# Kernel tuning notes

Hardware: AMD Instinct MI355X
Metric: run time of the kernel (lower is better)

Reference implementation:

```python
import jax, jax.numpy as jnp
import numpy as np
from jax import lax

N, E, F, H, B = 16384, 262144, 32, 128, 16
DI, DS, DC, DTR = 256, 16, 4, 8   # Mamba: d_inner=expand*H, d_state, d_conv, dt_rank=ceil(H/16)
NS, NC = 512, 8                   # num_stations, num line colors
EPS = 1e-5


def _forward(node_features, edge_index, batch, W_in, b_in, W_g1, b_g1, W_g2, b_g2,
             W_inproj, conv_w, conv_b, W_xproj, W_dt, b_dt, A_log, D_p, W_out,
             gamma, beta, Wc, bc, Wh, bh, Wt, bt, Wp1, bp1, Wp2, bp2, Wd, bd, Ws, bs):
    def gcn(x, W, b):
        # GCNConv with self-loops and symmetric normalization
        loops = jnp.arange(N)
        s = jnp.concatenate([edge_index[0], loops])
        d = jnp.concatenate([edge_index[1], loops])
        deg = jax.ops.segment_sum(jnp.ones(s.shape[0], x.dtype), d, num_segments=N)
        dinv = jnp.where(deg > 0, lax.rsqrt(deg), 0.0)
        xw = x @ W
        msg = xw[s] * (dinv[s] * dinv[d])[:, None]
        return jax.ops.segment_sum(msg, d, num_segments=N) + b

    h = jax.nn.relu(node_features @ W_in + b_in)
    h = jax.nn.relu(gcn(h, W_g1, b_g1))
    h_gnn = jax.nn.relu(gcn(h, W_g2, b_g2))

    # --- Mamba block over the node sequence (batch dim of 1, seq_len = N) ---
    xz = h_gnn @ W_inproj                      # (N, 2*DI)
    x, z = xz[:, :DI], xz[:, DI:]
    xp = jnp.pad(x, ((DC - 1, 0), (0, 0)))     # causal depthwise conv1d
    xc = conv_b + sum(xp[k:k + N] * conv_w[:, k] for k in range(DC))
    x = jax.nn.silu(xc)
    dbl = x @ W_xproj                          # (N, DTR + 2*DS)
    dt = jax.nn.softplus(dbl[:, :DTR] @ W_dt + b_dt)   # (N, DI)
    Bm = dbl[:, DTR:DTR + DS]                  # (N, DS)
    Cm = dbl[:, DTR + DS:]                     # (N, DS)
    A = -jnp.exp(A_log)                        # (DI, DS)
    dA = jnp.exp(dt[:, :, None] * A[None])     # (N, DI, DS)
    dBx = dt[:, :, None] * Bm[:, None, :] * x[:, :, None]

    def step(hst, t):
        dA_t, dBx_t, C_t = t
        hst = dA_t * hst + dBx_t               # (DI, DS)
        return hst, hst @ C_t                  # (DI,)

    _, ys = lax.scan(step, jnp.zeros((DI, DS), x.dtype), (dA, dBx, Cm))
    y = (ys + D_p * x) * jax.nn.silu(z)
    h_mamba = y @ W_out                        # (N, H)

    # residual + LayerNorm
    hh = h_gnn + h_mamba
    mu = hh.mean(-1, keepdims=True)
    var = ((hh - mu) ** 2).mean(-1, keepdims=True)
    h_final = (hh - mu) * lax.rsqrt(var + EPS) * gamma + beta

    # global_mean_pool per graph
    counts = jax.ops.segment_sum(jnp.ones(N, h_final.dtype), batch, num_segments=B)
    ge = jax.ops.segment_sum(h_final, batch, num_segments=B) / jnp.maximum(counts, 1.0)[:, None]

    # critic + all policy heads, concatenated: [1,4,3,NS,NS,NS,NC]
    return jnp.concatenate([ge @ Wc + bc, ge @ Wh + bh, ge @ Wt + bt,
                            ge @ Wp1 + bp1, ge @ Wp2 + bp2, ge @ Wd + bd,
                            ge @ Ws + bs], axis=-1)


def setup_inputs() -> dict:
    key = jax.random.key(0)
    ks = list(jax.random.split(key, 20))
    p = lambda i, shape, s=0.02: jax.random.normal(ks[i], shape, jnp.float32) * s
    return dict(
        node_features=jax.random.normal(ks[0], (N, F), jnp.float32),
        edge_index=jax.random.randint(ks[1], (2, E), 0, N),
        batch=jnp.sort(jax.random.randint(ks[2], (N,), 0, B)),
        W_in=p(3, (F, H)), b_in=jnp.zeros((H,), jnp.float32),
        W_g1=p(4, (H, H)), b_g1=jnp.zeros((H,), jnp.float32),
        W_g2=p(5, (H, H)), b_g2=jnp.zeros((H,), jnp.float32),
        W_inproj=p(6, (H, 2 * DI)),
        conv_w=p(7, (DI, DC)), conv_b=jnp.zeros((DI,), jnp.float32),
        W_xproj=p(8, (DI, DTR + 2 * DS)),
        W_dt=p(9, (DTR, DI)), b_dt=jnp.full((DI,), -4.0, jnp.float32),
        A_log=jnp.log(jnp.broadcast_to(jnp.arange(1.0, DS + 1.0, dtype=jnp.float32), (DI, DS))),
        D_p=jnp.ones((DI,), jnp.float32),
        W_out=p(10, (DI, H)),
        gamma=jnp.ones((H,), jnp.float32), beta=jnp.zeros((H,), jnp.float32),
        Wc=p(11, (H, 1)), bc=jnp.zeros((1,), jnp.float32),
        Wh=p(12, (H, 4)), bh=jnp.zeros((4,), jnp.float32),
        Wt=p(13, (H, 3)), bt=jnp.zeros((3,), jnp.float32),
        Wp1=p(14, (H, NS)), bp1=jnp.zeros((NS,), jnp.float32),
        Wp2=p(15, (H, NS)), bp2=jnp.zeros((NS,), jnp.float32),
        Wd=p(16, (H, NS)), bd=jnp.zeros((NS,), jnp.float32),
        Ws=p(17, (H, NC)), bs=jnp.zeros((NC,), jnp.float32),
    )


def reference(node_features, edge_index, batch, W_in, b_in, W_g1, b_g1, W_g2, b_g2,
              W_inproj, conv_w, conv_b, W_xproj, W_dt, b_dt, A_log, D_p, W_out,
              gamma, beta, Wc, bc, Wh, bh, Wt, bt, Wp1, bp1, Wp2, bp2, Wd, bd, Ws, bs):
    return _forward(node_features, edge_index, batch, W_in, b_in, W_g1, b_g1, W_g2, b_g2,
                    W_inproj, conv_w, conv_b, W_xproj, W_dt, b_dt, A_log, D_p, W_out,
                    gamma, beta, Wc, bc, Wh, bh, Wt, bt, Wp1, bp1, Wp2, bp2, Wd, bd, Ws, bs)
```

## Files before the change

### kernel.cpp

```cpp
#include <hip/hip_runtime.h>
#include <math.h>

#define NN 16384
#define EE 262144
#define FF 32
#define HH 128
#define BB 16
#define DI 256
#define DS 16
#define DC 4
#define DTR 8
#define OUTW 1552
#define NCH 256
#define CHLEN 64
#define NG 8
#define GL 32

__device__ __forceinline__ float siluf(float v) { return v / (1.f + __expf(-v)); }
__device__ __forceinline__ float softplusf(float v) {
    return fmaxf(v, 0.f) + __logf(1.f + __expf(-fabsf(v)));
}

__global__ void deg_kernel(const int* __restrict__ dst, int* __restrict__ cnt) {
    int e = blockIdx.x * blockDim.x + threadIdx.x;
    if (e < EE) atomicAdd(&cnt[dst[e]], 1);
}

__global__ __launch_bounds__(1024) void prefix_kernel(const int* __restrict__ cnt,
                                                      int* __restrict__ rowptr,
                                                      int* __restrict__ cursor,
                                                      float* __restrict__ dinv) {
    __shared__ int part[1024];
    int tid = threadIdx.x;
    int4 c4[4];
#pragma unroll
    for (int j = 0; j < 4; j++) c4[j] = ((const int4*)cnt)[tid * 4 + j];
    int v[16] = {c4[0].x, c4[0].y, c4[0].z, c4[0].w, c4[1].x, c4[1].y, c4[1].z, c4[1].w,
                 c4[2].x, c4[2].y, c4[2].z, c4[2].w, c4[3].x, c4[3].y, c4[3].z, c4[3].w};
    int s = 0;
#pragma unroll
    for (int j = 0; j < 16; j++) s += v[j];
    part[tid] = s;
    __syncthreads();
    for (int off = 1; off < 1024; off <<= 1) {
        int t = (tid >= off) ? part[tid - off] : 0;
        __syncthreads();
        part[tid] += t;
        __syncthreads();
    }
    int running = part[tid] - s;
    int rp[16];
    float dv[16];
#pragma unroll
    for (int j = 0; j < 16; j++) {
        rp[j] = running;
        running += v[j];
        dv[j] = rsqrtf((float)(v[j] + 1));
    }
#pragma unroll
    for (int j = 0; j < 4; j++) {
        int4 r4; r4.x = rp[j*4]; r4.y = rp[j*4+1]; r4.z = rp[j*4+2]; r4.w = rp[j*4+3];
        ((int4*)rowptr)[tid * 4 + j] = r4;
        ((int4*)cursor)[tid * 4 + j] = r4;
        float4 d4; d4.x = dv[j*4]; d4.y = dv[j*4+1]; d4.z = dv[j*4+2]; d4.w = dv[j*4+3];
        ((float4*)dinv)[tid * 4 + j] = d4;
    }
    if (tid == 1023) rowptr[NN] = part[1023];
}

__global__ void scatter_kernel(const int* __restrict__ src, const int* __restrict__ dst,
                               int* __restrict__ cursor, int* __restrict__ col) {
    int e = blockIdx.x * blockDim.x + threadIdx.x;
    if (e < EE) {
        int d = dst[e];
        int pos = atomicAdd(&cursor[d], 1);
        col[pos] = src[e];
    }
}

__global__ __launch_bounds__(256) void gemm_k(const float* __restrict__ A,
                                              const float* __restrict__ B,
                                              const float* __restrict__ bias,
                                              float* __restrict__ C,
                                              int M, int Nn, int K, int act) {
    __shared__ float As[16][68];
    __shared__ float Bs[16][68];
    int tid = threadIdx.x;
    int m0 = blockIdx.y * 64;
    int n0 = blockIdx.x * 64;
    int ty = tid >> 4, tx = tid & 15;
    float acc[4][4] = {{0.f}};
    for (int k0 = 0; k0 < K; k0 += 16) {
#pragma unroll
        for (int l = 0; l < 4; l++) {
            int idx = tid + l * 256;
            int i = idx >> 4, j = idx & 15;
            As[j][i] = A[(size_t)(m0 + i) * K + k0 + j];
        }
#pragma unroll
        for (int l = 0; l < 4; l++) {
            int idx = tid + l * 256;
            int i = idx >> 6, j = idx & 63;
            int n = n0 + j;
            Bs[i][j] = (n < Nn) ? B[(size_t)(k0 + i) * Nn + n] : 0.f;
        }
        __syncthreads();
#pragma unroll
        for (int kk = 0; kk < 16; kk++) {
            float4 a4 = *(const float4*)&As[kk][ty * 4];
            float4 b4 = *(const float4*)&Bs[kk][tx * 4];
            float av[4] = {a4.x, a4.y, a4.z, a4.w};
            float bv[4] = {b4.x, b4.y, b4.z, b4.w};
#pragma unroll
            for (int r = 0; r < 4; r++)
#pragma unroll
                for (int c = 0; c < 4; c++) acc[r][c] = fmaf(av[r], bv[c], acc[r][c]);
        }
        __syncthreads();
    }
    int nb = n0 + tx * 4;
    if (nb < Nn) {
        float4 bi4 = {0.f, 0.f, 0.f, 0.f};
        if (bias) bi4 = *(const float4*)&bias[nb];
#pragma unroll
        for (int r = 0; r < 4; r++) {
            int m = m0 + ty * 4 + r;
            float4 v;
            v.x = acc[r][0] + bi4.x; v.y = acc[r][1] + bi4.y;
            v.z = acc[r][2] + bi4.z; v.w = acc[r][3] + bi4.w;
            if (act == 1) {
                v.x = fmaxf(v.x, 0.f); v.y = fmaxf(v.y, 0.f);
                v.z = fmaxf(v.z, 0.f); v.w = fmaxf(v.w, 0.f);
            }
            *(float4*)&C[(size_t)m * Nn + nb] = v;
        }
    }
}

__global__ __launch_bounds__(256, 4) void gemm_big(const float* __restrict__ A,
                                                   const float* __restrict__ B,
                                                   float* __restrict__ C,
                                                   int M, int Nn, int K) {
    __shared__ float As[16][132];
    __shared__ float Bs[16][132];
    int tid = threadIdx.x;
    int m0 = blockIdx.y * 128;
    int n0 = blockIdx.x * 128;
    int ty = tid >> 4, tx = tid & 15;
    float acc[8][8] = {{0.f}};
    for (int k0 = 0; k0 < K; k0 += 16) {
        {
            int m = tid >> 1;
            int kc = (tid & 1) * 8;
            const float* ap = &A[(size_t)(m0 + m) * K + k0 + kc];
            float4 a0 = *(const float4*)ap;
            float4 a1 = *(const float4*)(ap + 4);
            As[kc + 0][m] = a0.x; As[kc + 1][m] = a0.y;
            As[kc + 2][m] = a0.z; As[kc + 3][m] = a0.w;
            As[kc + 4][m] = a1.x; As[kc + 5][m] = a1.y;
            As[kc + 6][m] = a1.z; As[kc + 7][m] = a1.w;
        }
        {
            int krow = tid >> 4;
            int c8 = (tid & 15) * 8;
            const float* bp = &B[(size_t)(k0 + krow) * Nn + n0 + c8];
            *(float4*)&Bs[krow][c8] = *(const float4*)bp;
            *(float4*)&Bs[krow][c8 + 4] = *(const float4*)(bp + 4);
        }
        __syncthreads();
#pragma unroll
        for (int kk = 0; kk < 16; kk++) {
            float4 a0 = *(const float4*)&As[kk][ty * 4];
            float4 a1 = *(const float4*)&As[kk][64 + ty * 4];
            float4 b0 = *(const float4*)&Bs[kk][tx * 4];
            float4 b1 = *(const float4*)&Bs[kk][64 + tx * 4];
            float av[8] = {a0.x, a0.y, a0.z, a0.w, a1.x, a1.y, a1.z, a1.w};
            float bv[8] = {b0.x, b0.y, b0.z, b0.w, b1.x, b1.y, b1.z, b1.w};
#pragma unroll
            for (int r = 0; r < 8; r++)
#pragma unroll
                for (int c = 0; c < 8; c++) acc[r][c] = fmaf(av[r], bv[c], acc[r][c]);
        }
        __syncthreads();
    }
#pragma unroll
    for (int r = 0; r < 8; r++) {
        int m = m0 + ((r < 4) ? (ty * 4 + r) : (64 + ty * 4 + r - 4));
        float4 v0, v1;
        v0.x = acc[r][0]; v0.y = acc[r][1]; v0.z = acc[r][2]; v0.w = acc[r][3];
        v1.x = acc[r][4]; v1.y = acc[r][5]; v1.z = acc[r][6]; v1.w = acc[r][7];
        *(float4*)&C[(size_t)m * Nn + n0 + tx * 4] = v0;
        *(float4*)&C[(size_t)m * Nn + n0 + 64 + tx * 4] = v1;
    }
}

__global__ __launch_bounds__(256) void gemm_at(const float* __restrict__ AT,
                                               const float* __restrict__ B,
                                               float* __restrict__ C,
                                               int M, int Nn, int K) {
    __shared__ float As[16][68];
    __shared__ float Bs[16][68];
    int tid = threadIdx.x;
    int m0 = blockIdx.y * 64;
    int n0 = blockIdx.x * 64;
    int ty = tid >> 4, tx = tid & 15;
    float acc[4][4] = {{0.f}};
    for (int k0 = 0; k0 < K; k0 += 16) {
#pragma unroll
        for (int l = 0; l < 4; l++) {
            int idx = tid + l * 256;
            int kk = idx >> 6, i = idx & 63;
            As[kk][i] = AT[(size_t)(k0 + kk) * M + m0 + i];
        }
#pragma unroll
        for (int l = 0; l < 4; l++) {
            int idx = tid + l * 256;
            int i = idx >> 6, j = idx & 63;
            int n = n0 + j;
            Bs[i][j] = (n < Nn) ? B[(size_t)(k0 + i) * Nn + n] : 0.f;
        }
        __syncthreads();
#pragma unroll
        for (int kk = 0; kk < 16; kk++) {
            float4 a4 = *(const float4*)&As[kk][ty * 4];
            float4 b4 = *(const float4*)&Bs[kk][tx * 4];
            float av[4] = {a4.x, a4.y, a4.z, a4.w};
            float bv[4] = {b4.x, b4.y, b4.z, b4.w};
#pragma unroll
            for (int r = 0; r < 4; r++)
#pragma unroll
                for (int c = 0; c < 4; c++) acc[r][c] = fmaf(av[r], bv[c], acc[r][c]);
        }
        __syncthreads();
    }
    int nb = n0 + tx * 4;
    if (nb < Nn) {
#pragma unroll
        for (int r = 0; r < 4; r++) {
            int m = m0 + ty * 4 + r;
            float4 v;
            v.x = acc[r][0]; v.y = acc[r][1]; v.z = acc[r][2]; v.w = acc[r][3];
            *(float4*)&C[(size_t)m * Nn + nb] = v;
        }
    }
}

__global__ __launch_bounds__(256) void gemm_at_ln(const float* __restrict__ AT,
                                                  const float* __restrict__ B,
                                                  const float* __restrict__ hg,
                                                  const float* __restrict__ gamma,
                                                  const float* __restrict__ beta,
                                                  float* __restrict__ out) {
    __shared__ float As[16][68];
    __shared__ float Bs[16][132];
    int tid = threadIdx.x;
    int m0 = blockIdx.x * 64;
    int ty = tid >> 4, tx = tid & 15;
    float acc[4][8] = {{0.f}};
    for (int k0 = 0; k0 < 256; k0 += 16) {
#pragma unroll
        for (int l = 0; l < 4; l++) {
            int idx = tid + l * 256;
            int kk = idx >> 6, i = idx & 63;
            As[kk][i] = AT[(size_t)(k0 + kk) * NN + m0 + i];
        }
        {
            int krow = tid >> 4;
            int c8 = (tid & 15) * 8;
            const float* bp = &B[(size_t)(k0 + krow) * HH + c8];
            *(float4*)&Bs[krow][c8] = *(const float4*)bp;
            *(float4*)&Bs[krow][c8 + 4] = *(const float4*)(bp + 4);
        }
        __syncthreads();
#pragma unroll
        for (int kk = 0; kk < 16; kk++) {
            float4 a4 = *(const float4*)&As[kk][ty * 4];
            float4 b0 = *(const float4*)&Bs[kk][tx * 4];
            float4 b1 = *(const float4*)&Bs[kk][64 + tx * 4];
            float av[4] = {a4.x, a4.y, a4.z, a4.w};
            float bv[8] = {b0.x, b0.y, b0.z, b0.w, b1.x, b1.y, b1.z, b1.w};
#pragma unroll
            for (int r = 0; r < 4; r++)
#pragma unroll
                for (int c = 0; c < 8; c++) acc[r][c] = fmaf(av[r], bv[c], acc[r][c]);
        }
        __syncthreads();
    }
    float4 g0 = *(const float4*)&gamma[tx * 4];
    float4 g1 = *(const float4*)&gamma[64 + tx * 4];
    float4 be0 = *(const float4*)&beta[tx * 4];
    float4 be1 = *(const float4*)&beta[64 + tx * 4];
    float gv[8] = {g0.x, g0.y, g0.z, g0.w, g1.x, g1.y, g1.z, g1.w};
    float bv[8] = {be0.x, be0.y, be0.z, be0.w, be1.x, be1.y, be1.z, be1.w};
#pragma unroll
    for (int r = 0; r < 4; r++) {
        int m = m0 + ty * 4 + r;
        float4 h0 = *(const float4*)&hg[(size_t)m * HH + tx * 4];
        float4 h1 = *(const float4*)&hg[(size_t)m * HH + 64 + tx * 4];
        float v[8] = {acc[r][0] + h0.x, acc[r][1] + h0.y, acc[r][2] + h0.z, acc[r][3] + h0.w,
                      acc[r][4] + h1.x, acc[r][5] + h1.y, acc[r][6] + h1.z, acc[r][7] + h1.w};
        float sum = 0.f;
#pragma unroll
        for (int c = 0; c < 8; c++) sum += v[c];
        sum += __shfl_xor(sum, 1); sum += __shfl_xor(sum, 2);
        sum += __shfl_xor(sum, 4); sum += __shfl_xor(sum, 8);
        float mu = sum * (1.f / 128.f);
        float vs = 0.f;
#pragma unroll
        for (int c = 0; c < 8; c++) { float dd = v[c] - mu; vs += dd * dd; }
        vs += __shfl_xor(vs, 1); vs += __shfl_xor(vs, 2);
        vs += __shfl_xor(vs, 4); vs += __shfl_xor(vs, 8);
        float inv = rsqrtf(vs * (1.f / 128.f) + 1e-5f);
        float4 o0, o1;
        o0.x = (v[0] - mu) * inv * gv[0] + bv[0];
        o0.y = (v[1] - mu) * inv * gv[1] + bv[1];
        o0.z = (v[2] - mu) * inv * gv[2] + bv[2];
        o0.w = (v[3] - mu) * inv * gv[3] + bv[3];
        o1.x = (v[4] - mu) * inv * gv[4] + bv[4];
        o1.y = (v[5] - mu) * inv * gv[5] + bv[5];
        o1.z = (v[6] - mu) * inv * gv[6] + bv[6];
        o1.w = (v[7] - mu) * inv * gv[7] + bv[7];
        *(float4*)&out[(size_t)m * HH + tx * 4] = o0;
        *(float4*)&out[(size_t)m * HH + 64 + tx * 4] = o1;
    }
}

__global__ __launch_bounds__(256) void gcn_gather4(const float* __restrict__ xw,
                                                   const int* __restrict__ rowptr,
                                                   const int* __restrict__ col,
                                                   const float* __restrict__ dinv,
                                                   const float* __restrict__ b,
                                                   float* __restrict__ out) {
    int tid = threadIdx.x;
    int sub = tid & 31;
    int n = blockIdx.x * 8 + (tid >> 5);
    float dn = dinv[n];
    const float4* xw4 = (const float4*)xw;
    float4 a = xw4[(size_t)n * 32 + sub];
    float ws = dn * dn;
    float4 acc;
    acc.x = a.x * ws; acc.y = a.y * ws; acc.z = a.z * ws; acc.w = a.w * ws;
    int beg = rowptr[n], end = rowptr[n + 1];
    int e = beg;
    for (; e + 2 <= end; e += 2) {
        int s0 = col[e], s1 = col[e + 1];
        float w0 = dinv[s0] * dn, w1 = dinv[s1] * dn;
        float4 v0 = xw4[(size_t)s0 * 32 + sub];
        float4 v1 = xw4[(size_t)s1 * 32 + sub];
        acc.x = fmaf(v0.x, w0, acc.x); acc.y = fmaf(v0.y, w0, acc.y);
        acc.z = fmaf(v0.z, w0, acc.z); acc.w = fmaf(v0.w, w0, acc.w);
        acc.x = fmaf(v1.x, w1, acc.x); acc.y = fmaf(v1.y, w1, acc.y);
        acc.z = fmaf(v1.z, w1, acc.z); acc.w = fmaf(v1.w, w1, acc.w);
    }
    if (e < end) {
        int s0 = col[e];
        float w0 = dinv[s0] * dn;
        float4 v0 = xw4[(size_t)s0 * 32 + sub];
        acc.x = fmaf(v0.x, w0, acc.x); acc.y = fmaf(v0.y, w0, acc.y);
        acc.z = fmaf(v0.z, w0, acc.z); acc.w = fmaf(v0.w, w0, acc.w);
    }
    float4 b4 = ((const float4*)b)[sub];
    acc.x = fmaxf(acc.x + b4.x, 0.f);
    acc.y = fmaxf(acc.y + b4.y, 0.f);
    acc.z = fmaxf(acc.z + b4.z, 0.f);
    acc.w = fmaxf(acc.w + b4.w, 0.f);
    ((float4*)out)[(size_t)n * 32 + sub] = acc;
}

__global__ __launch_bounds__(256) void conv_silu_t(const float* __restrict__ xz,
                                                   const float* __restrict__ cw,
                                                   const float* __restrict__ cb,
                                                   float* __restrict__ xst,
                                                   float* __restrict__ szt) {
    __shared__ float tile[67][65];
    int tid = threadIdx.x;
    int t0 = blockIdx.x * 64;
    int c0 = blockIdx.y * 64;
#pragma unroll
    for (int l = 0; l < 17; l++) {
        int idx = tid + l * 256;
        if (idx < 67 * 64) {
            int r = idx >> 6, c = idx & 63;
            int gt = t0 - 3 + r;
            tile[r][c] = (gt >= 0) ? xz[(size_t)gt * 512 + c0 + c] : 0.f;
        }
    }
    __syncthreads();
    int tl = tid & 63;
    int d0 = tid >> 6;
    if (c0 < 256) {
#pragma unroll
        for (int l = 0; l < 16; l++) {
            int dl = d0 + l * 4;
            int dg = c0 + dl;
            float acc = cb[dg];
#pragma unroll
            for (int k = 0; k < DC; k++)
                acc = fmaf(tile[tl + k][dl], cw[dg * DC + k], acc);
            xst[dg * NN + t0 + tl] = siluf(acc);
        }
    } else {
#pragma unroll
        for (int l = 0; l < 16; l++) {
            int dl = d0 + l * 4;
            int dg = c0 - 256 + dl;
            szt[dg * NN + t0 + tl] = siluf(tile[tl + 3][dl]);
        }
    }
}

__global__ __launch_bounds__(256) void transpose_dbl(const float* __restrict__ dbl,
                                                     float* __restrict__ dblt) {
    __shared__ float tile[64][41];
    int tid = threadIdx.x;
    int t0 = blockIdx.x * 64;
#pragma unroll
    for (int l = 0; l < 10; l++) {
        int idx = tid + l * 256;
        int r = idx / 40, c = idx - r * 40;
        tile[r][c] = dbl[(size_t)(t0 + r) * 40 + c];
    }
    __syncthreads();
#pragma unroll
    for (int l = 0; l < 10; l++) {
        int idx = tid + l * 256;
        int c = idx >> 6, t = idx & 63;
        dblt[c * NN + t0 + t] = tile[t][c];
    }
}

__global__ __launch_bounds__(256, 6) void scan_phase1(const float* __restrict__ xst,
                                                      const float* __restrict__ dblt,
                                                      const float* __restrict__ A_log,
                                                      const float* __restrict__ W_dt,
                                                      const float* __restrict__ b_dt,
                                                      float* __restrict__ chkP,
                                                      float* __restrict__ chkH) {
    __shared__ float Td[32][68];
    __shared__ float Tx[32][68];
    __shared__ float Bs[16][68];
    __shared__ float D8[8][68];
    int tid = threadIdx.x;
    int wave = tid >> 6, lane = tid & 63;
    int sg = lane & 7, dl = lane >> 3;
    int dblk = blockIdx.x, chunk = blockIdx.y;
    int t0 = chunk * CHLEN;
    int dloc = wave * 8 + dl;
    int d = dblk * 32 + dloc;
    int s0 = 2 * sg;
#pragma unroll
    for (int p = 0; p < 2; p++) {
        int linear = tid + p * 256;
        int row = linear >> 4, c4 = (linear & 15) * 4;
        *(float4*)&Tx[row][c4] = *(const float4*)&xst[(size_t)(dblk * 32 + row) * NN + t0 + c4];
    }
    if (tid < 128) {
        int r = tid >> 4, c4 = (tid & 15) * 4;
        *(float4*)&D8[r][c4] = *(const float4*)&dblt[(size_t)r * NN + t0 + c4];
    }
    {
        int s = tid >> 4, c4 = (tid & 15) * 4;
        *(float4*)&Bs[s][c4] = *(const float4*)&dblt[(size_t)(8 + s) * NN + t0 + c4];
    }
    float A0 = -expf(A_log[d * DS + s0]);
    float A1 = -expf(A_log[d * DS + s0 + 1]);
    __syncthreads();
    {
        int row = tid >> 3;
        int tb = (tid & 7) * 8;
        int dd = dblk * 32 + row;
        float bd = b_dt[dd];
        float wv[8];
#pragma unroll
        for (int j = 0; j < 8; j++) wv[j] = W_dt[j * DI + dd];
#pragma unroll
        for (int j = 0; j < 8; j++) {
            int t = tb + j;
            float acc = bd;
#pragma unroll
            for (int k = 0; k < 8; k++) acc = fmaf(D8[k][t], wv[k], acc);
            Td[row][t] = softplusf(acc);
        }
    }
    __syncthreads();
    float h0 = 0.f, h1 = 0.f, P0 = 1.f, P1 = 1.f;
    for (int i = 0; i < CHLEN; i += 4) {
        float4 d4 = *(const float4*)&Td[dloc][i];
        float4 x4 = *(const float4*)&Tx[dloc][i];
        float4 b04 = *(const float4*)&Bs[s0][i];
        float4 b14 = *(const float4*)&Bs[s0 + 1][i];
#define P1S(U) { float dtv = d4.U; float a0 = __expf(dtv * A0); float a1 = __expf(dtv * A1); \
        float dx = dtv * x4.U; h0 = fmaf(a0, h0, dx * b04.U); h1 = fmaf(a1, h1, dx * b14.U); \
        P0 *= a0; P1 *= a1; }
        P1S(x) P1S(y) P1S(z) P1S(w)
#undef P1S
    }
    int idx = chunk * 4096 + d * DS + s0;
    float2 vP; vP.x = P0; vP.y = P1;
    float2 vH; vH.x = h0; vH.y = h1;
    *(float2*)(chkP + idx) = vP;
    *(float2*)(chkH + idx) = vH;
}

__global__ void scan_phase2a(const float* __restrict__ chkP, const float* __restrict__ chkH,
                             float* __restrict__ gp, float* __restrict__ gh) {
    int g = blockIdx.x * blockDim.x + threadIdx.x;
    int idx = g & 4095;
    int grp = g >> 12;
    int c0 = grp * GL;
    float P = 1.f, H = 0.f;
    for (int j = 0; j < GL; j += 4) {
        float p[4], q[4];
#pragma unroll
        for (int jj = 0; jj < 4; jj++) {
            p[jj] = chkP[(c0 + j + jj) * 4096 + idx];
            q[jj] = chkH[(c0 + j + jj) * 4096 + idx];
        }
#pragma unroll
        for (int jj = 0; jj < 4; jj++) {
            H = fmaf(p[jj], H, q[jj]);
            P *= p[jj];
        }
    }
    gp[grp * 4096 + idx] = P;
    gh[grp * 4096 + idx] = H;
}

__global__ void scan_phase2b(const float* __restrict__ gp, const float* __restrict__ gh,
                             float* __restrict__ gini) {
    int idx = blockIdx.x * blockDim.x + threadIdx.x;
    float h = 0.f;
#pragma unroll
    for (int g = 0; g < NG; g++) {
        gini[g * 4096 + idx] = h;
        h = fmaf(gp[g * 4096 + idx], h, gh[g * 4096 + idx]);
    }
}

__global__ void scan_phase2c(const float* __restrict__ chkP, const float* __restrict__ chkH,
                             const float* __restrict__ gini, float* __restrict__ init) {
    int g = blockIdx.x * blockDim.x + threadIdx.x;
    int idx = g & 4095;
    int grp = g >> 12;
    int c0 = grp * GL;
    float h = gini[grp * 4096 + idx];
    for (int j = 0; j < GL; j += 4) {
        float p[4], q[4];
#pragma unroll
        for (int jj = 0; jj < 4; jj++) {
            p[jj] = chkP[(c0 + j + jj) * 4096 + idx];
            q[jj] = chkH[(c0 + j + jj) * 4096 + idx];
        }
#pragma unroll
        for (int jj = 0; jj < 4; jj++) {
            init[(c0 + j + jj) * 4096 + idx] = h;
            h = fmaf(p[jj], h, q[jj]);
        }
    }
}

__global__ __launch_bounds__(256, 5) void scan_phase3(const float* __restrict__ xst,
                                                      const float* __restrict__ dblt,
                                                      const float* __restrict__ A_log,
                                                      const float* __restrict__ W_dt,
                                                      const float* __restrict__ b_dt,
                                                      const float* __restrict__ init,
                                                      const float* __restrict__ D_p,
                                                      const float* __restrict__ szt,
                                                      float* __restrict__ yt) {
    __shared__ float Td[32][68];
    __shared__ float Tx[32][68];
    __shared__ float Bs[16][68];
    __shared__ float Cs[16][68];
    __shared__ float D8[8][68];
    int tid = threadIdx.x;
    int wave = tid >> 6, lane = tid & 63;
    int sg = lane & 7, dl = lane >> 3;
    int dblk = blockIdx.x, chunk = blockIdx.y;
    int t0 = chunk * CHLEN;
    int dloc = wave * 8 + dl;
    int d = dblk * 32 + dloc;
    int s0 = 2 * sg;
#pragma unroll
    for (int p = 0; p < 2; p++) {
        int linear = tid + p * 256;
        int row = linear >> 4, c4 = (linear & 15) * 4;
        *(float4*)&Tx[row][c4] = *(const float4*)&xst[(size_t)(dblk * 32 + row) * NN + t0 + c4];
    }
    if (tid < 128) {
        int r = tid >> 4, c4 = (tid & 15) * 4;
        *(float4*)&D8[r][c4] = *(const float4*)&dblt[(size_t)r * NN + t0 + c4];
    }
    {
        int s = tid >> 4, c4 = (tid & 15) * 4;
        *(float4*)&Bs[s][c4] = *(const float4*)&dblt[(size_t)(8 + s) * NN + t0 + c4];
        *(float4*)&Cs[s][c4] = *(const float4*)&dblt[(size_t)(24 + s) * NN + t0 + c4];
    }
    float A0 = -expf(A_log[d * DS + s0]);
    float A1 = -expf(A_log[d * DS + s0 + 1]);
    float Dd = D_p[d];
    float2 ini = *(const float2*)(init + chunk * 4096 + d * DS + s0);
    float h0 = ini.x, h1 = ini.y;
    __syncthreads();
    {
        int row = tid >> 3;
        int tb = (tid & 7) * 8;
        int dd = dblk * 32 + row;
        float bd = b_dt[dd];
        float wv[8];
#pragma unroll
        for (int j = 0; j < 8; j++) wv[j] = W_dt[j * DI + dd];
#pragma unroll
        for (int j = 0; j < 8; j++) {
            int t = tb + j;
            float acc = bd;
#pragma unroll
            for (int k = 0; k < 8; k++) acc = fmaf(D8[k][t], wv[k], acc);
            Td[row][t] = softplusf(acc);
        }
    }
    __syncthreads();
    for (int i = 0; i < CHLEN; i += 4) {
        float4 d4 = *(const float4*)&Td[dloc][i];
        float4 x4 = *(const float4*)&Tx[dloc][i];
        float4 b04 = *(const float4*)&Bs[s0][i];
        float4 b14 = *(const float4*)&Bs[s0 + 1][i];
        float4 c04 = *(const float4*)&Cs[s0][i];
        float4 c14 = *(const float4*)&Cs[s0 + 1][i];
        float4 yv;
#define P3S(U) { float dtv = d4.U; float a0 = __expf(dtv * A0); float a1 = __expf(dtv * A1); \
        float dx = dtv * x4.U; h0 = fmaf(a0, h0, dx * b04.U); h1 = fmaf(a1, h1, dx * b14.U); \
        float c = fmaf(h1, c14.U, h0 * c04.U); \
        c += __shfl_xor(c, 1); c += __shfl_xor(c, 2); c += __shfl_xor(c, 4); \
        yv.U = c + Dd * x4.U; }
        P3S(x) P3S(y) P3S(z) P3S(w)
#undef P3S
        if (sg == 0) *(float4*)&Td[dloc][i] = yv;
    }
#pragma unroll
    for (int r = 0; r < 8; r++) {
        int row = wave * 8 + r;
        float sz = szt[(size_t)(dblk * 32 + row) * NN + t0 + lane];
        yt[(size_t)(dblk * 32 + row) * NN + t0 + lane] = Td[row][lane] * sz;
    }
}

__global__ void pool_kernel(const float* __restrict__ hf, const int* __restrict__ batch,
                            float* __restrict__ ge, int* __restrict__ counts) {
    int f = threadIdx.x;
    int r0 = blockIdx.x * 128;
    int gcur = batch[r0];
    float acc = 0.f;
    int cnt = 0;
    for (int i = 0; i < 128; i += 4) {
        int r = r0 + i;
        int g0 = batch[r], g3 = batch[r + 3];
        float v0 = hf[(size_t)r * HH + f];
        float v1 = hf[(size_t)(r + 1) * HH + f];
        float v2 = hf[(size_t)(r + 2) * HH + f];
        float v3 = hf[(size_t)(r + 3) * HH + f];
        if (g0 == gcur && g3 == gcur) {
            acc += (v0 + v1) + (v2 + v3);
            cnt += 4;
        } else {
            int gs[4] = {g0, batch[r + 1], batch[r + 2], g3};
            float vs[4] = {v0, v1, v2, v3};
#pragma unroll
            for (int k = 0; k < 4; k++) {
                if (gs[k] != gcur) {
                    atomicAdd(&ge[gcur * HH + f], acc);
                    if (f == 0) atomicAdd(&counts[gcur], cnt);
                    acc = 0.f; cnt = 0; gcur = gs[k];
                }
                acc += vs[k];
                cnt++;
            }
        }
    }
    atomicAdd(&ge[gcur * HH + f], acc);
    if (f == 0) atomicAdd(&counts[gcur], cnt);
}

__global__ void heads_kernel(const float* __restrict__ ge, const int* __restrict__ counts,
                             const float* Wc, const float* bc, const float* Wh, const float* bh,
                             const float* Wt, const float* bt, const float* Wp1, const float* bp1,
                             const float* Wp2, const float* bp2, const float* Wd, const float* bd,
                             const float* Ws, const float* bs, float* __restrict__ out) {
    int col = blockIdx.x * blockDim.x + threadIdx.x;
    int b = blockIdx.y;
    if (col >= OUTW) return;
    const float* W; const float* bi; int lc, w;
    if (col < 1)         { W = Wc;  bi = bc;  lc = col;        w = 1; }
    else if (col < 5)    { W = Wh;  bi = bh;  lc = col - 1;    w = 4; }
    else if (col < 8)    { W = Wt;  bi = bt;  lc = col - 5;    w = 3; }
    else if (col < 520)  { W = Wp1; bi = bp1; lc = col - 8;    w = 512; }
    else if (col < 1032) { W = Wp2; bi = bp2; lc = col - 520;  w = 512; }
    else if (col < 1544) { W = Wd;  bi = bd;  lc = col - 1032; w = 512; }
    else                 { W = Ws;  bi = bs;  lc = col - 1544; w = 8; }
    float scale = 1.f / fmaxf((float)counts[b], 1.f);
    float dot = 0.f;
#pragma unroll 8
    for (int f = 0; f < HH; f++) dot = fmaf(ge[b * HH + f], W[f * w + lc], dot);
    out[(size_t)b * OUTW + col] = bi[lc] + scale * dot;
}

extern "C" void kernel_launch(void* const* d_in, const int* in_sizes, int n_in,
                              void* d_out, int out_size, void* d_ws, size_t ws_size,
                              hipStream_t stream) {
    const float* nf      = (const float*)d_in[0];
    const int*   ei      = (const int*)d_in[1];
    const int*   batch   = (const int*)d_in[2];
    const float* W_in    = (const float*)d_in[3];
    const float* b_in    = (const float*)d_in[4];
    const float* W_g1    = (const float*)d_in[5];
    const float* b_g1    = (const float*)d_in[6];
    const float* W_g2    = (const float*)d_in[7];
    const float* b_g2    = (const float*)d_in[8];
    const float* W_inproj= (const float*)d_in[9];
    const float* conv_w  = (const float*)d_in[10];
    const float* conv_b  = (const float*)d_in[11];
    const float* W_xproj = (const float*)d_in[12];
    const float* W_dt    = (const float*)d_in[13];
    const float* b_dt    = (const float*)d_in[14];
    const float* A_log   = (const float*)d_in[15];
    const float* D_p     = (const float*)d_in[16];
    const float* W_out   = (const float*)d_in[17];
    const float* gamma   = (const float*)d_in[18];
    const float* beta    = (const float*)d_in[19];
    const float* Wc = (const float*)d_in[20]; const float* bc = (const float*)d_in[21];
    const float* Wh = (const float*)d_in[22]; const float* bh = (const float*)d_in[23];
    const float* Wt = (const float*)d_in[24]; const float* bt = (const float*)d_in[25];
    const float* Wp1= (const float*)d_in[26]; const float* bp1= (const float*)d_in[27];
    const float* Wp2= (const float*)d_in[28]; const float* bp2= (const float*)d_in[29];
    const float* Wd = (const float*)d_in[30]; const float* bd = (const float*)d_in[31];
    const float* Ws = (const float*)d_in[32]; const float* bs = (const float*)d_in[33];

    const int* e_src = ei;
    const int* e_dst = ei + EE;

    float* w = (float*)d_ws;
    size_t o = 0;
    float* F0   = w + o; o += (size_t)NN * HH;
    float* F1   = w + o; o += (size_t)NN * HH;
    float* F2   = w + o; o += (size_t)NN * HH;
    float* XZ   = w + o; o += (size_t)NN * 512;
    float* YT   = XZ;
    float* XST  = w + o; o += (size_t)NN * DI;
    float* SZT  = w + o; o += (size_t)NN * DI;
    float* DBL  = w + o; o += (size_t)NN * 40;
    float* DBLT = w + o; o += (size_t)NN * 40;
    float* GE   = w + o; o += BB * HH;
    float* DINV = w + o; o += NN;
    int* ip = (int*)(w + o);
    int* CNT    = ip; ip += NN;
    int* ROWPTR = ip; ip += NN + 1;
    int* CURSOR = ip; ip += NN;
    int* COL    = ip; ip += EE;
    int* COUNTS = ip; ip += BB;

    float* CHP  = F0;
    float* CHH  = F0 + (size_t)NCH * 4096;
    float* INI  = F1;
    float* GP   = DBL;
    float* GH   = DBL + NG * 4096;
    float* GINI = DBL + 2 * NG * 4096;

    hipMemsetAsync(CNT, 0, NN * sizeof(int), stream);
    hipMemsetAsync(GE, 0, BB * HH * sizeof(float), stream);
    hipMemsetAsync(COUNTS, 0, BB * sizeof(int), stream);

    deg_kernel<<<EE / 256, 256, 0, stream>>>(e_dst, CNT);
    prefix_kernel<<<1, 1024, 0, stream>>>(CNT, ROWPTR, CURSOR, DINV);
    scatter_kernel<<<EE / 256, 256, 0, stream>>>(e_src, e_dst, CURSOR, COL);

    gemm_k<<<dim3(2, NN / 64), 256, 0, stream>>>(nf, W_in, b_in, F0, NN, HH, FF, 1);
    gemm_k<<<dim3(2, NN / 64), 256, 0, stream>>>(F0, W_g1, nullptr, F1, NN, HH, HH, 0);
    gcn_gather4<<<NN / 8, 256, 0, stream>>>(F1, ROWPTR, COL, DINV, b_g1, F0);
    gemm_k<<<dim3(2, NN / 64), 256, 0, stream>>>(F0, W_g2, nullptr, F1, NN, HH, HH, 0);
    gcn_gather4<<<NN / 8, 256, 0, stream>>>(F1, ROWPTR, COL, DINV, b_g2, F2);

    gemm_big<<<dim3(4, NN / 128), 256, 0, stream>>>(F2, W_inproj, XZ, NN, 512, HH);
    conv_silu_t<<<dim3(NN / 64, 8), 256, 0, stream>>>(XZ, conv_w, conv_b, XST, SZT);
    gemm_at<<<dim3(1, NN / 64), 256, 0, stream>>>(XST, W_xproj, DBL, NN, 40, DI);
    transpose_dbl<<<NN / 64, 256, 0, stream>>>(DBL, DBLT);

    scan_phase1<<<dim3(8, NCH), 256, 0, stream>>>(XST, DBLT, A_log, W_dt, b_dt, CHP, CHH);
    scan_phase2a<<<(4096 * NG) / 256, 256, 0, stream>>>(CHP, CHH, GP, GH);
    scan_phase2b<<<16, 256, 0, stream>>>(GP, GH, GINI);
    scan_phase2c<<<(4096 * NG) / 256, 256, 0, stream>>>(CHP, CHH, GINI, INI);
    scan_phase3<<<dim3(8, NCH), 256, 0, stream>>>(XST, DBLT, A_log, W_dt, b_dt, INI, D_p, SZT, YT);

    gemm_at_ln<<<NN / 64, 256, 0, stream>>>(YT, W_out, F2, gamma, beta, F0);

    pool_kernel<<<NN / 128, HH, 0, stream>>>(F0, batch, GE, COUNTS);

    heads_kernel<<<dim3((OUTW + 127) / 128, BB), 128, 0, stream>>>(
        GE, COUNTS, Wc, bc, Wh, bh, Wt, bt, Wp1, bp1, Wp2, bp2, Wd, bd, Ws, bs, (float*)d_out);
}
```

Measured before the change: 425.3 us.

## Fuse xproj transpose into GEMM, merge scan phases, retile LN GEMM, unroll gather

The x_proj GEMM now writes its output transposed through a shared-memory tile, so the separate transpose kernel and its intermediate buffer go away. The group-prefix kernel scan_phase2b is folded into scan_phase2c, where each thread recomputes its group's initial state with a short serial loop. The output-projection+LayerNorm GEMM uses 32-row tiles, giving twice as many blocks but less reuse per block. The GCN gather loop is unrolled by four to keep more loads in flight. Together these cut two kernel launches and one round trip through global memory, at the cost of some redundant work in the scan.

```diff
diff --git a/kernel.cpp b/kernel.cpp
--- a/kernel.cpp
+++ b/kernel.cpp
@@ -194,30 +194,28 @@
     }
 }
 
-__global__ __launch_bounds__(256) void gemm_at(const float* __restrict__ AT,
-                                               const float* __restrict__ B,
-                                               float* __restrict__ C,
-                                               int M, int Nn, int K) {
+__global__ __launch_bounds__(256) void gemm_at_dblt(const float* __restrict__ AT,
+                                                    const float* __restrict__ B,
+                                                    float* __restrict__ dblt) {
     __shared__ float As[16][68];
     __shared__ float Bs[16][68];
-    int tid = threadIdx.x;
-    int m0 = blockIdx.y * 64;
-    int n0 = blockIdx.x * 64;
+    __shared__ float Ct[64][41];
+    int tid = threadIdx.x;
+    int m0 = blockIdx.x * 64;
     int ty = tid >> 4, tx = tid & 15;
     float acc[4][4] = {{0.f}};
-    for (int k0 = 0; k0 < K; k0 += 16) {
+    for (int k0 = 0; k0 < DI; k0 += 16) {
 #pragma unroll
         for (int l = 0; l < 4; l++) {
             int idx = tid + l * 256;
             int kk = idx >> 6, i = idx & 63;
-            As[kk][i] = AT[(size_t)(k0 + kk) * M + m0 + i];
+            As[kk][i] = AT[(size_t)(k0 + kk) * NN + m0 + i];
         }
 #pragma unroll
         for (int l = 0; l < 4; l++) {
             int idx = tid + l * 256;
             int i = idx >> 6, j = idx & 63;
-            int n = n0 + j;
-            Bs[i][j] = (n < Nn) ? B[(size_t)(k0 + i) * Nn + n] : 0.f;
+            Bs[i][j] = (j < 40) ? B[(size_t)(k0 + i) * 40 + j] : 0.f;
         }
         __syncthreads();
 #pragma unroll
@@ -233,15 +231,22 @@
         }
         __syncthreads();
     }
-    int nb = n0 + tx * 4;
-    if (nb < Nn) {
+    if (tx * 4 < 40) {
 #pragma unroll
         for (int r = 0; r < 4; r++) {
-            int m = m0 + ty * 4 + r;
-            float4 v;
-            v.x = acc[r][0]; v.y = acc[r][1]; v.z = acc[r][2]; v.w = acc[r][3];
-            *(float4*)&C[(size_t)m * Nn + nb] = v;
-        }
+            int m = ty * 4 + r;
+            Ct[m][tx * 4 + 0] = acc[r][0];
+            Ct[m][tx * 4 + 1] = acc[r][1];
+            Ct[m][tx * 4 + 2] = acc[r][2];
+            Ct[m][tx * 4 + 3] = acc[r][3];
+        }
+    }
+    __syncthreads();
+#pragma unroll
+    for (int l = 0; l < 10; l++) {
+        int idx = tid + l * 256;
+        int n = idx >> 6, m = idx & 63;
+        dblt[(size_t)n * NN + m0 + m] = Ct[m][n];
     }
 }
 
@@ -251,18 +256,18 @@
                                                   const float* __restrict__ gamma,
                                                   const float* __restrict__ beta,
                                                   float* __restrict__ out) {
-    __shared__ float As[16][68];
+    __shared__ float As[16][36];
     __shared__ float Bs[16][132];
     int tid = threadIdx.x;
-    int m0 = blockIdx.x * 64;
+    int m0 = blockIdx.x * 32;
     int ty = tid >> 4, tx = tid & 15;
-    float acc[4][8] = {{0.f}};
+    float acc[2][8] = {{0.f}};
     for (int k0 = 0; k0 < 256; k0 += 16) {
-#pragma unroll
-        for (int l = 0; l < 4; l++) {
-            int idx = tid + l * 256;
-            int kk = idx >> 6, i = idx & 63;
+        {
+            int idx = tid * 2;
+            int kk = idx >> 5, i = idx & 31;
             As[kk][i] = AT[(size_t)(k0 + kk) * NN + m0 + i];
+            As[kk][i + 1] = AT[(size_t)(k0 + kk) * NN + m0 + i + 1];
         }
         {
             int krow = tid >> 4;
@@ -274,15 +279,16 @@
         __syncthreads();
 #pragma unroll
         for (int kk = 0; kk < 16; kk++) {
-            float4 a4 = *(const float4*)&As[kk][ty * 4];
+            float a0 = As[kk][ty * 2];
+            float a1 = As[kk][ty * 2 + 1];
             float4 b0 = *(const float4*)&Bs[kk][tx * 4];
             float4 b1 = *(const float4*)&Bs[kk][64 + tx * 4];
-            float av[4] = {a4.x, a4.y, a4.z, a4.w};
             float bv[8] = {b0.x, b0.y, b0.z, b0.w, b1.x, b1.y, b1.z, b1.w};
 #pragma unroll
-            for (int r = 0; r < 4; r++)
-#pragma unroll
-                for (int c = 0; c < 8; c++) acc[r][c] = fmaf(av[r], bv[c], acc[r][c]);
+            for (int c = 0; c < 8; c++) {
+                acc[0][c] = fmaf(a0, bv[c], acc[0][c]);
+                acc[1][c] = fmaf(a1, bv[c], acc[1][c]);
+            }
         }
         __syncthreads();
     }
@@ -293,8 +299,8 @@
     float gv[8] = {g0.x, g0.y, g0.z, g0.w, g1.x, g1.y, g1.z, g1.w};
     float bv[8] = {be0.x, be0.y, be0.z, be0.w, be1.x, be1.y, be1.z, be1.w};
 #pragma unroll
-    for (int r = 0; r < 4; r++) {
-        int m = m0 + ty * 4 + r;
+    for (int r = 0; r < 2; r++) {
+        int m = m0 + ty * 2 + r;
         float4 h0 = *(const float4*)&hg[(size_t)m * HH + tx * 4];
         float4 h1 = *(const float4*)&hg[(size_t)m * HH + 64 + tx * 4];
         float v[8] = {acc[r][0] + h0.x, acc[r][1] + h0.y, acc[r][2] + h0.z, acc[r][3] + h0.w,
@@ -342,17 +348,24 @@
     acc.x = a.x * ws; acc.y = a.y * ws; acc.z = a.z * ws; acc.w = a.w * ws;
     int beg = rowptr[n], end = rowptr[n + 1];
     int e = beg;
-    for (; e + 2 <= end; e += 2) {
-        int s0 = col[e], s1 = col[e + 1];
+    for (; e + 4 <= end; e += 4) {
+        int s0 = col[e], s1 = col[e + 1], s2 = col[e + 2], s3 = col[e + 3];
         float w0 = dinv[s0] * dn, w1 = dinv[s1] * dn;
+        float w2 = dinv[s2] * dn, w3 = dinv[s3] * dn;
         float4 v0 = xw4[(size_t)s0 * 32 + sub];
         float4 v1 = xw4[(size_t)s1 * 32 + sub];
+        float4 v2 = xw4[(size_t)s2 * 32 + sub];
+        float4 v3 = xw4[(size_t)s3 * 32 + sub];
         acc.x = fmaf(v0.x, w0, acc.x); acc.y = fmaf(v0.y, w0, acc.y);
         acc.z = fmaf(v0.z, w0, acc.z); acc.w = fmaf(v0.w, w0, acc.w);
         acc.x = fmaf(v1.x, w1, acc.x); acc.y = fmaf(v1.y, w1, acc.y);
         acc.z = fmaf(v1.z, w1, acc.z); acc.w = fmaf(v1.w, w1, acc.w);
-    }
-    if (e < end) {
+        acc.x = fmaf(v2.x, w2, acc.x); acc.y = fmaf(v2.y, w2, acc.y);
+        acc.z = fmaf(v2.z, w2, acc.z); acc.w = fmaf(v2.w, w2, acc.w);
+        acc.x = fmaf(v3.x, w3, acc.x); acc.y = fmaf(v3.y, w3, acc.y);
+        acc.z = fmaf(v3.z, w3, acc.z); acc.w = fmaf(v3.w, w3, acc.w);
+    }
+    for (; e < end; e++) {
         int s0 = col[e];
         float w0 = dinv[s0] * dn;
         float4 v0 = xw4[(size_t)s0 * 32 + sub];
@@ -406,26 +419,6 @@
             int dg = c0 - 256 + dl;
             szt[dg * NN + t0 + tl] = siluf(tile[tl + 3][dl]);
         }
-    }
-}
-
-__global__ __launch_bounds__(256) void transpose_dbl(const float* __restrict__ dbl,
-                                                     float* __restrict__ dblt) {
-    __shared__ float tile[64][41];
-    int tid = threadIdx.x;
-    int t0 = blockIdx.x * 64;
-#pragma unroll
-    for (int l = 0; l < 10; l++) {
-        int idx = tid + l * 256;
-        int r = idx / 40, c = idx - r * 40;
-        tile[r][c] = dbl[(size_t)(t0 + r) * 40 + c];
-    }
-    __syncthreads();
-#pragma unroll
-    for (int l = 0; l < 10; l++) {
-        int idx = tid + l * 256;
-        int c = idx >> 6, t = idx & 63;
-        dblt[c * NN + t0 + t] = tile[t][c];
     }
 }
 
@@ -526,24 +519,16 @@
     gh[grp * 4096 + idx] = H;
 }
 
-__global__ void scan_phase2b(const float* __restrict__ gp, const float* __restrict__ gh,
-                             float* __restrict__ gini) {
-    int idx = blockIdx.x * blockDim.x + threadIdx.x;
-    float h = 0.f;
-#pragma unroll
-    for (int g = 0; g < NG; g++) {
-        gini[g * 4096 + idx] = h;
-        h = fmaf(gp[g * 4096 + idx], h, gh[g * 4096 + idx]);
-    }
-}
-
 __global__ void scan_phase2c(const float* __restrict__ chkP, const float* __restrict__ chkH,
-                             const float* __restrict__ gini, float* __restrict__ init) {
+                             const float* __restrict__ gp, const float* __restrict__ gh,
+                             float* __restrict__ init) {
     int g = blockIdx.x * blockDim.x + threadIdx.x;
     int idx = g & 4095;
     int grp = g >> 12;
     int c0 = grp * GL;
-    float h = gini[grp * 4096 + idx];
+    float h = 0.f;
+    for (int gg = 0; gg < grp; gg++)
+        h = fmaf(gp[gg * 4096 + idx], h, gh[gg * 4096 + idx]);
     for (int j = 0; j < GL; j += 4) {
         float p[4], q[4];
 #pragma unroll
@@ -763,7 +748,6 @@
     float* INI  = F1;
     float* GP   = DBL;
     float* GH   = DBL + NG * 4096;
-    float* GINI = DBL + 2 * NG * 4096;
 
     hipMemsetAsync(CNT, 0, NN * sizeof(int), stream);
     hipMemsetAsync(GE, 0, BB * HH * sizeof(float), stream);
@@ -781,16 +765,14 @@
 
     gemm_big<<<dim3(4, NN / 128), 256, 0, stream>>>(F2, W_inproj, XZ, NN, 512, HH);
     conv_silu_t<<<dim3(NN / 64, 8), 256, 0, stream>>>(XZ, conv_w, conv_b, XST, SZT);
-    gemm_at<<<dim3(1, NN / 64), 256, 0, stream>>>(XST, W_xproj, DBL, NN, 40, DI);
-    transpose_dbl<<<NN / 64, 256, 0, stream>>>(DBL, DBLT);
+    gemm_at_dblt<<<NN / 64, 256, 0, stream>>>(XST, W_xproj, DBLT);
 
     scan_phase1<<<dim3(8, NCH), 256, 0, stream>>>(XST, DBLT, A_log, W_dt, b_dt, CHP, CHH);
     scan_phase2a<<<(4096 * NG) / 256, 256, 0, stream>>>(CHP, CHH, GP, GH);
-    scan_phase2b<<<16, 256, 0, stream>>>(GP, GH, GINI);
-    scan_phase2c<<<(4096 * NG) / 256, 256, 0, stream>>>(CHP, CHH, GINI, INI);
+    scan_phase2c<<<(4096 * NG) / 256, 256, 0, stream>>>(CHP, CHH, GP, GH, INI);
     scan_phase3<<<dim3(8, NCH), 256, 0, stream>>>(XST, DBLT, A_log, W_dt, b_dt, INI, D_p, SZT, YT);
 
-    gemm_at_ln<<<NN / 64, 256, 0, stream>>>(YT, W_out, F2, gamma, beta, F0);
+    gemm_at_ln<<<NN / 32, 256, 0, stream>>>(YT, W_out, F2, gamma, beta, F0);
 
     pool_kernel<<<NN / 128, HH, 0, stream>>>(F0, batch, GE, COUNTS);
 
```

Measured after the change: 412.8 us. 1.03x faster.
